# Kernel optimization log

Hardware: AMD Instinct MI355X
Metric: run time of the kernel (lower is better)

Reference implementation:

```python
import jax, jax.numpy as jnp
import numpy as np

B, L_IN, D_MODEL, CONV_D, KSIZE = 16, 512, 384, 1536, 3
MEL_MAX = 4096
LN_EPS = 1e-5


def _conv1d_same(h, w, b):
    # h: [B, C_in, L], w: [C_out, C_in, K] -> [B, C_out, L]
    y = jax.lax.conv_general_dilated(h, w, window_strides=(1,), padding='SAME',
                                     dimension_numbers=('NCH', 'OIH', 'NCH'))
    return y + b[None, :, None]


def _layernorm(x, g, b):
    m = jnp.mean(x, -1, keepdims=True)
    v = jnp.mean((x - m) ** 2, -1, keepdims=True)
    return (x - m) * jax.lax.rsqrt(v + LN_EPS) * g + b


def _ffn(x, wa, ba, wb, bb):
    # Conv1D_FFT: conv(d_model->conv_d) ReLU conv(conv_d->d_model) ReLU
    h = jnp.transpose(x, (0, 2, 1))
    h = jax.nn.relu(_conv1d_same(h, wa, ba))
    h = jax.nn.relu(_conv1d_same(h, wb, bb))
    return jnp.transpose(h, (0, 2, 1))


def _dur_pred(x, w1, b1, w2, b2, g1, be1, w3, b3, w4, b4, g2, be2, wl, bl):
    h = _ffn(x, w1, b1, w2, b2)
    h = _layernorm(h, g1, be1)  # dropout is identity at eval
    h = _ffn(h, w3, b3, w4, b4)
    h = _layernorm(h, g2, be2)
    return (h @ wl + bl)[..., 0]  # [B, L_in], squeeze(-1)


def _length_regulate(x, dur, mel_max_len):
    # Equivalent to alignment @ x where alignment[b,t,j]=1 iff cum[b,j-1] <= t < cum[b,j],
    # padded with zeros out to mel_max_len (original pads output to mel_max_len).
    cum = jnp.cumsum(dur, axis=-1)                        # [B, L_in]
    total = cum[:, -1]                                    # [B]
    t = jnp.arange(mel_max_len, dtype=cum.dtype)          # [T]
    idx = jax.vmap(lambda c: jnp.searchsorted(c, t, side='right'))(cum)  # [B, T]
    idx = jnp.minimum(idx, x.shape[1] - 1)
    out = jnp.take_along_axis(x, idx[:, :, None], axis=1)  # [B, T, D]
    mask = (t[None, :] < total[:, None])[..., None]
    return out * mask


def setup_inputs() -> dict:
    key = jax.random.key(0)
    ks = jax.random.split(key, 8)
    def nrm(k, shape):
        return jax.random.normal(k, shape, jnp.float32) * 0.02
    return {
        'x': jax.random.normal(ks[0], (B, L_IN, D_MODEL), jnp.float32),
        'target': jax.random.randint(ks[1], (B, L_IN), 0, 8, jnp.int32),
        'mel_max_len': MEL_MAX,
        'w1': nrm(ks[2], (CONV_D, D_MODEL, KSIZE)), 'b1': jnp.zeros((CONV_D,), jnp.float32),
        'w2': nrm(ks[3], (D_MODEL, CONV_D, KSIZE)), 'b2': jnp.zeros((D_MODEL,), jnp.float32),
        'g1': jnp.ones((D_MODEL,), jnp.float32), 'be1': jnp.zeros((D_MODEL,), jnp.float32),
        'w3': nrm(ks[4], (CONV_D, D_MODEL, KSIZE)), 'b3': jnp.zeros((CONV_D,), jnp.float32),
        'w4': nrm(ks[5], (D_MODEL, CONV_D, KSIZE)), 'b4': jnp.zeros((D_MODEL,), jnp.float32),
        'g2': jnp.ones((D_MODEL,), jnp.float32), 'be2': jnp.zeros((D_MODEL,), jnp.float32),
        'wl': nrm(ks[6], (D_MODEL, 1)), 'bl': jnp.zeros((1,), jnp.float32),
    }


def reference(x, target, mel_max_len, w1, b1, w2, b2, g1, be1, w3, b3, w4, b4, g2, be2, wl, bl):
    dur_preds = _dur_pred(x, w1, b1, w2, b2, g1, be1, w3, b3, w4, b4, g2, be2, wl, bl)
    output = _length_regulate(x, target, mel_max_len)
    return (output, dur_preds)
```

## Files before the change

### kernel.cpp

```cpp
#include <hip/hip_runtime.h>
#include <hip/hip_bf16.h>
#include <cstddef>
#include <cstdint>

#define NB 16
#define LIN 512
#define DM 384
#define DC 1536
#define MELMAX 4096
#define LN_EPS 1e-5f

typedef __bf16 bf16x8 __attribute__((ext_vector_type(8)));
typedef float f32x4 __attribute__((ext_vector_type(4)));

#define GL2LDS(gp, lp)                                                                \
    __builtin_amdgcn_global_load_lds((const __attribute__((address_space(1))) void*)(gp), \
                                     (__attribute__((address_space(3))) void*)(lp), 16, 0, 0)

__device__ __forceinline__ float wred(float v) {
#pragma unroll
    for (int m = 32; m >= 1; m >>= 1) v += __shfl_xor(v, m, 64);
    return v;
}

__device__ __forceinline__ unsigned short f2bf(float f) {
    __hip_bfloat16 h = __float2bfloat16(f);
    return *reinterpret_cast<unsigned short*>(&h);
}

__device__ __forceinline__ float bf2f(unsigned short u) {
    return __uint_as_float(((unsigned)u) << 16);
}


__global__ void cumsum_kernel(const int* __restrict__ tgt, int* __restrict__ cum) {
    __shared__ int s[LIN];
    const int b = blockIdx.x, tid = threadIdx.x;
    s[tid] = tgt[b * LIN + tid];
    __syncthreads();
    for (int off = 1; off < LIN; off <<= 1) {
        int v = (tid >= off) ? s[tid - off] : 0;
        __syncthreads();
        s[tid] += v;
        __syncthreads();
    }
    cum[b * LIN + tid] = s[tid];
}


__global__ __launch_bounds__(256) void gather_kernel(const float* __restrict__ x,
                                                     const int* __restrict__ cum,
                                                     float* __restrict__ out) {
    const int wid = (blockIdx.x * 256 + threadIdx.x) >> 6;
    const int lane = threadIdx.x & 63;
    const int b = wid >> 12;
    const int t = wid & (MELMAX - 1);
    const int* c = cum + b * LIN;
    const int total = c[LIN - 1];
    float4* orow = reinterpret_cast<float4*>(out + ((size_t)b * MELMAX + t) * DM);
    if (t < total) {
        int lo = 0, hi = LIN;
        while (lo < hi) { int mid = (lo + hi) >> 1; if (c[mid] > t) hi = mid; else lo = mid + 1; }
        const int idx = lo < (LIN - 1) ? lo : (LIN - 1);
        const float4* xrow = reinterpret_cast<const float4*>(x + ((size_t)b * LIN + idx) * DM);
#pragma unroll
        for (int j = 0; j < 2; ++j) {
            const int p = lane + 64 * j;
            if (p < DM / 4) orow[p] = xrow[p];
        }
    } else {
        const float4 z = make_float4(0.f, 0.f, 0.f, 0.f);
#pragma unroll
        for (int j = 0; j < 2; ++j) {
            const int p = lane + 64 * j;
            if (p < DM / 4) orow[p] = z;
        }
    }
}


__global__ void zpad_kernel(unsigned short* __restrict__ p, int rowlen) {
    const int b = blockIdx.x >> 1;
    const int row = (blockIdx.x & 1) ? (LIN + 1) : 0;
    unsigned short* base = p + ((size_t)b * (LIN + 2) + row) * rowlen;
    for (int c = threadIdx.x; c < rowlen; c += 256) base[c] = 0;
}

__global__ void cast_x_kernel(const float* __restrict__ x, unsigned short* __restrict__ xb) {
    const int idx = blockIdx.x * 256 + threadIdx.x;
    const int total = NB * LIN * DM / 4;
    if (idx >= total) return;
    const float4 v = reinterpret_cast<const float4*>(x)[idx];
    const int e = idx * 4;
    const int b = e / (LIN * DM);
    const int rem = e - b * (LIN * DM);
    const int l = rem / DM;
    const int c = rem - l * DM;
    ushort4 o;
    o.x = f2bf(v.x); o.y = f2bf(v.y); o.z = f2bf(v.z); o.w = f2bf(v.w);
    *reinterpret_cast<ushort4*>(xb + ((size_t)b * (LIN + 2) + l + 1) * DM + c) = o;
}

template <int CI, int CO>
__global__ void wcast_kernel(const float* __restrict__ w, unsigned short* __restrict__ wg) {
    const int idx = blockIdx.x * 256 + threadIdx.x;
    if (idx >= CO * CI) return;
    const int co = idx / CI;
    const int ci = idx - co * CI;
    const float* p = w + (size_t)idx * 3;
    unsigned short* o = wg + (size_t)co * (3 * CI) + ci;
    o[0 * CI] = f2bf(p[0]);
    o[1 * CI] = f2bf(p[1]);
    o[2 * CI] = f2bf(p[2]);
}


template <int CI, int CO, int BN>
__global__ __launch_bounds__(256, 2) void conv_mfma_kernel(const unsigned short* __restrict__ in,
                                                           const unsigned short* __restrict__ wg,
                                                           const float* __restrict__ bias,
                                                           unsigned short* __restrict__ out) {
    constexpr int BM = 128, BK = 32;
    constexpr int KC = CI / BK;
    constexpr int AROWS = BM + 16;
    constexpr int AGRP = AROWS / 16;
    constexpr int BGRP = 3 * BN / 16;
    constexpr int GPT = BN / 16;
    constexpr int NW_N = BN / 32;
    constexpr int NT = CO / BN;
    constexpr int MT = LIN / BM;

    __shared__ __align__(16) unsigned short As[AROWS * BK];
    __shared__ __align__(16) unsigned short Bs[3 * BN * BK];

    const int orig = blockIdx.x, nwg = gridDim.x;
    const int q = nwg >> 3, r = nwg & 7, xcd = orig & 7, o = orig >> 3;
    const int wgid = (xcd < r ? xcd * (q + 1) : r * (q + 1) + (xcd - r) * q) + o;

    const int mg = wgid / NT;
    const int nt = wgid - mg * NT;
    const int b = mg >> 2;
    const int l0 = (mg & (MT - 1)) * BM;
    const int n0 = nt * BN;

    const int tid = threadIdx.x;
    const int lane = tid & 63;
    const int wv = tid >> 6;
    const int wr = wv >> 1, wc = wv & 1;

    const unsigned short* inb = in + (size_t)b * (LIN + 2) * CI;

    f32x4 acc[4][NW_N];
#pragma unroll
    for (int m = 0; m < 4; ++m)
#pragma unroll
        for (int n = 0; n < NW_N; ++n) acc[m][n] = (f32x4){0.f, 0.f, 0.f, 0.f};

    const int lrow = lane >> 2;
    const int lch = lane & 3;

    for (int kb = 0; kb < KC; ++kb) {
        const int kin = kb * BK;
        const unsigned short* abase = inb + (size_t)l0 * CI + kin + lch * 8;
        for (int g = wv; g < AGRP; g += 4) {
            GL2LDS(abase + (size_t)(g * 16 + lrow) * CI, As + g * 512);
        }
        for (int g2 = wv; g2 < BGRP; g2 += 4) {
            const int t = g2 / GPT, gr = g2 - t * GPT;
            const unsigned short* gb =
                wg + (size_t)(n0 + gr * 16 + lrow) * (3 * CI) + (size_t)t * CI + kin + lch * 8;
            GL2LDS(gb, Bs + g2 * 512);
        }
        __syncthreads();
        {
            const int fr = lane & 15, kg = lane >> 4;
#pragma unroll
            for (int t = 0; t < 3; ++t) {
                bf16x8 aF[4], bF[NW_N];
#pragma unroll
                for (int m = 0; m < 4; ++m)
                    aF[m] = *reinterpret_cast<const bf16x8*>(
                        As + (t + wr * 64 + m * 16 + fr) * BK + kg * 8);
#pragma unroll
                for (int n = 0; n < NW_N; ++n)
                    bF[n] = *reinterpret_cast<const bf16x8*>(
                        Bs + ((size_t)t * BN + wc * (BN / 2) + n * 16 + fr) * BK + kg * 8);
#pragma unroll
                for (int m = 0; m < 4; ++m)
#pragma unroll
                    for (int n = 0; n < NW_N; ++n)
                        acc[m][n] = __builtin_amdgcn_mfma_f32_16x16x32_bf16(aF[m], bF[n], acc[m][n], 0, 0, 0);
            }
        }
        __syncthreads();
    }

    const int fr = lane & 15, fq = lane >> 4;
    float bv[NW_N];
#pragma unroll
    for (int n = 0; n < NW_N; ++n) bv[n] = bias[n0 + wc * (BN / 2) + n * 16 + fr];
    unsigned short* outb = out + (size_t)b * (LIN + 2) * CO;
#pragma unroll
    for (int m = 0; m < 4; ++m)
#pragma unroll
        for (int qy = 0; qy < 4; ++qy) {
            const int grow = l0 + wr * 64 + m * 16 + fq * 4 + qy + 1;
            unsigned short* orow = outb + (size_t)grow * CO + n0 + wc * (BN / 2) + fr;
#pragma unroll
            for (int n = 0; n < NW_N; ++n) {
                const float v = fmaxf(acc[m][n][qy] + bv[n], 0.f);
                orow[n * 16] = f2bf(v);
            }
        }
}


__global__ void ln_kernel(unsigned short* __restrict__ h, const float* __restrict__ g,
                          const float* __restrict__ be) {
    const int row = blockIdx.x, lane = threadIdx.x;
    const int b = row >> 9, l = row & (LIN - 1);
    unsigned short* hr = h + ((size_t)b * (LIN + 2) + l + 1) * DM;
    float v[6];
    float s = 0.f;
#pragma unroll
    for (int j = 0; j < 6; ++j) { v[j] = bf2f(hr[lane + 64 * j]); s += v[j]; }
    s = wred(s);
    const float mean = s * (1.f / DM);
    float vs = 0.f;
#pragma unroll
    for (int j = 0; j < 6; ++j) { const float d = v[j] - mean; vs += d * d; }
    vs = wred(vs);
    const float rstd = rsqrtf(vs * (1.f / DM) + LN_EPS);
#pragma unroll
    for (int j = 0; j < 6; ++j) {
        const int c = lane + 64 * j;
        hr[c] = f2bf((v[j] - mean) * rstd * g[c] + be[c]);
    }
}


__global__ void ln_linear_kernel(const unsigned short* __restrict__ h, const float* __restrict__ g,
                                 const float* __restrict__ be, const float* __restrict__ wl,
                                 const float* __restrict__ bl, float* __restrict__ dur) {
    const int row = blockIdx.x, lane = threadIdx.x;
    const int b = row >> 9, l = row & (LIN - 1);
    const unsigned short* hr = h + ((size_t)b * (LIN + 2) + l + 1) * DM;
    float v[6];
    float s = 0.f;
#pragma unroll
    for (int j = 0; j < 6; ++j) { v[j] = bf2f(hr[lane + 64 * j]); s += v[j]; }
    s = wred(s);
    const float mean = s * (1.f / DM);
    float vs = 0.f;
#pragma unroll
    for (int j = 0; j < 6; ++j) { const float d = v[j] - mean; vs += d * d; }
    vs = wred(vs);
    const float rstd = rsqrtf(vs * (1.f / DM) + LN_EPS);
    float dot = 0.f;
#pragma unroll
    for (int j = 0; j < 6; ++j) {
        const int c = lane + 64 * j;
        dot += ((v[j] - mean) * rstd * g[c] + be[c]) * wl[c];
    }
    dot = wred(dot);
    if (lane == 0) dur[row] = dot + bl[0];
}


extern "C" void kernel_launch(void* const* d_in, const int* in_sizes, int n_in,
                              void* d_out, int out_size, void* d_ws, size_t ws_size,
                              hipStream_t stream) {
    const float* x   = (const float*)d_in[0];
    const int*   tgt = (const int*)d_in[1];
    const float* w1  = (const float*)d_in[3];
    const float* b1  = (const float*)d_in[4];
    const float* w2  = (const float*)d_in[5];
    const float* b2  = (const float*)d_in[6];
    const float* g1  = (const float*)d_in[7];
    const float* be1 = (const float*)d_in[8];
    const float* w3  = (const float*)d_in[9];
    const float* b3  = (const float*)d_in[10];
    const float* w4  = (const float*)d_in[11];
    const float* b4  = (const float*)d_in[12];
    const float* g2  = (const float*)d_in[13];
    const float* be2 = (const float*)d_in[14];
    const float* wl  = (const float*)d_in[15];
    const float* bl  = (const float*)d_in[16];

    float* out = (float*)d_out;
    float* dur = out + (size_t)NB * MELMAX * DM;

    unsigned short* ws = (unsigned short*)d_ws;
    unsigned short* xb   = ws;
    unsigned short* hbig = xb + (size_t)NB * (LIN + 2) * DM;
    unsigned short* h2b  = hbig + (size_t)NB * (LIN + 2) * DC;
    unsigned short* wg1  = h2b + (size_t)NB * (LIN + 2) * DM;
    unsigned short* wg2  = wg1 + (size_t)DC * 3 * DM;
    unsigned short* wg3  = wg2 + (size_t)DM * 3 * DC;
    unsigned short* wg4  = wg3 + (size_t)DC * 3 * DM;
    int* cum = (int*)(wg4 + (size_t)DM * 3 * DC);

    cumsum_kernel<<<NB, LIN, 0, stream>>>(tgt, cum);
    gather_kernel<<<(NB * MELMAX) / 4, 256, 0, stream>>>(x, cum, out);

    zpad_kernel<<<NB * 2, 256, 0, stream>>>(xb, DM);
    zpad_kernel<<<NB * 2, 256, 0, stream>>>(hbig, DC);
    zpad_kernel<<<NB * 2, 256, 0, stream>>>(h2b, DM);
    cast_x_kernel<<<(NB * LIN * DM / 4 + 255) / 256, 256, 0, stream>>>(x, xb);
    wcast_kernel<DM, DC><<<(DC * DM + 255) / 256, 256, 0, stream>>>(w1, wg1);
    wcast_kernel<DC, DM><<<(DM * DC + 255) / 256, 256, 0, stream>>>(w2, wg2);
    wcast_kernel<DM, DC><<<(DC * DM + 255) / 256, 256, 0, stream>>>(w3, wg3);
    wcast_kernel<DC, DM><<<(DM * DC + 255) / 256, 256, 0, stream>>>(w4, wg4);

    conv_mfma_kernel<DM, DC, 128><<<NB * (LIN / 128) * (DC / 128), 256, 0, stream>>>(xb, wg1, b1, hbig);
    conv_mfma_kernel<DC, DM, 64><<<NB * (LIN / 128) * (DM / 64), 256, 0, stream>>>(hbig, wg2, b2, h2b);
    ln_kernel<<<NB * LIN, 64, 0, stream>>>(h2b, g1, be1);
    conv_mfma_kernel<DM, DC, 128><<<NB * (LIN / 128) * (DC / 128), 256, 0, stream>>>(h2b, wg3, b3, hbig);
    conv_mfma_kernel<DC, DM, 64><<<NB * (LIN / 128) * (DM / 64), 256, 0, stream>>>(hbig, wg4, b4, xb);
    ln_linear_kernel<<<NB * LIN, 64, 0, stream>>>(xb, g2, be2, wl, bl, dur);
}
```

Before: 242.6 us.

## Double-buffer LDS tiles in conv MFMA kernel and merge setup launches

The conv MFMA kernel now keeps two LDS buffers for the A and B tiles, so global-to-LDS loads for the next K block are issued before computing on the current one, and one of the two barriers per K step is removed. The three zero-pad launches and the four weight-cast launches are each merged into a single kernel to cut launch overhead. Double buffering doubles LDS use per block, which may lower occupancy below the two blocks per CU the launch bounds target.

```diff
diff --git a/kernel.cpp b/kernel.cpp
--- a/kernel.cpp
+++ b/kernel.cpp
@@ -79,11 +79,15 @@
 }
 
 
-__global__ void zpad_kernel(unsigned short* __restrict__ p, int rowlen) {
-    const int b = blockIdx.x >> 1;
-    const int row = (blockIdx.x & 1) ? (LIN + 1) : 0;
-    unsigned short* base = p + ((size_t)b * (LIN + 2) + row) * rowlen;
-    for (int c = threadIdx.x; c < rowlen; c += 256) base[c] = 0;
+__global__ void zpad3_kernel(unsigned short* __restrict__ xb, unsigned short* __restrict__ hb,
+                             unsigned short* __restrict__ h2) {
+    const int i = blockIdx.x;
+    const int buf = i >> 5, rem = i & 31;
+    const int b = rem >> 1, row = (rem & 1) ? (LIN + 1) : 0;
+    unsigned short* p = buf == 0 ? xb : (buf == 1 ? hb : h2);
+    const int rl = buf == 1 ? DC : DM;
+    unsigned short* base = p + ((size_t)b * (LIN + 2) + row) * rl;
+    for (int c = threadIdx.x; c < rl; c += 256) base[c] = 0;
 }
 
 __global__ void cast_x_kernel(const float* __restrict__ x, unsigned short* __restrict__ xb) {
@@ -101,14 +105,19 @@
     *reinterpret_cast<ushort4*>(xb + ((size_t)b * (LIN + 2) + l + 1) * DM + c) = o;
 }
 
-template <int CI, int CO>
-__global__ void wcast_kernel(const float* __restrict__ w, unsigned short* __restrict__ wg) {
+__global__ void wcast_all_kernel(const float* __restrict__ w1, const float* __restrict__ w2,
+                                 const float* __restrict__ w3, const float* __restrict__ w4,
+                                 unsigned short* __restrict__ o1, unsigned short* __restrict__ o2,
+                                 unsigned short* __restrict__ o3, unsigned short* __restrict__ o4) {
     const int idx = blockIdx.x * 256 + threadIdx.x;
-    if (idx >= CO * CI) return;
-    const int co = idx / CI;
-    const int ci = idx - co * CI;
+    if (idx >= DC * DM) return;
+    const int which = blockIdx.y;
+    const float* w = which == 0 ? w1 : which == 1 ? w2 : which == 2 ? w3 : w4;
+    unsigned short* gg = which == 0 ? o1 : which == 1 ? o2 : which == 2 ? o3 : o4;
+    const int CI = (which == 0 || which == 2) ? DM : DC;
+    const int co = idx / CI, ci = idx - co * CI;
     const float* p = w + (size_t)idx * 3;
-    unsigned short* o = wg + (size_t)co * (3 * CI) + ci;
+    unsigned short* o = gg + (size_t)co * (3 * CI) + ci;
     o[0 * CI] = f2bf(p[0]);
     o[1 * CI] = f2bf(p[1]);
     o[2 * CI] = f2bf(p[2]);
@@ -124,14 +133,14 @@
     constexpr int KC = CI / BK;
     constexpr int AROWS = BM + 16;
     constexpr int AGRP = AROWS / 16;
-    constexpr int BGRP = 3 * BN / 16;
     constexpr int GPT = BN / 16;
+    constexpr int BGRP = 3 * GPT;
     constexpr int NW_N = BN / 32;
     constexpr int NT = CO / BN;
     constexpr int MT = LIN / BM;
 
-    __shared__ __align__(16) unsigned short As[AROWS * BK];
-    __shared__ __align__(16) unsigned short Bs[3 * BN * BK];
+    __shared__ __align__(16) unsigned short As[2][AROWS * BK];
+    __shared__ __align__(16) unsigned short Bs[2][3 * BN * BK];
 
     const int orig = blockIdx.x, nwg = gridDim.x;
     const int q = nwg >> 3, r = nwg & 7, xcd = orig & 7, o = orig >> 3;
@@ -158,44 +167,64 @@
 
     const int lrow = lane >> 2;
     const int lch = lane & 3;
-
-    for (int kb = 0; kb < KC; ++kb) {
-        const int kin = kb * BK;
-        const unsigned short* abase = inb + (size_t)l0 * CI + kin + lch * 8;
-        for (int g = wv; g < AGRP; g += 4) {
-            GL2LDS(abase + (size_t)(g * 16 + lrow) * CI, As + g * 512);
+    const int fr = lane & 15, kg = lane >> 4;
+
+    const unsigned short* aroot = inb + (size_t)l0 * CI + lch * 8;
+    const unsigned short* broot = wg + (size_t)n0 * (3 * CI) + lch * 8;
+
+#define STAGE(c, kb)                                                                      \
+    do {                                                                                  \
+        const unsigned short* abase = aroot + (kb) * BK;                                  \
+        for (int g = wv; g < AGRP; g += 4)                                                \
+            GL2LDS(abase + (size_t)(g * 16 + lrow) * CI, &As[c][g * 512]);                \
+        const unsigned short* bbase = broot + (kb) * BK;                                  \
+        for (int g2 = wv; g2 < BGRP; g2 += 4) {                                           \
+            const int t = g2 / GPT, gr = g2 - t * GPT;                                    \
+            GL2LDS(bbase + (size_t)(gr * 16 + lrow) * (3 * CI) + (size_t)t * CI,          \
+                   &Bs[c][g2 * 512]);                                                     \
+        }                                                                                 \
+    } while (0)
+
+#define COMPUTE(c)                                                                        \
+    do {                                                                                  \
+        _Pragma("unroll")                                                                 \
+        for (int t = 0; t < 3; ++t) {                                                     \
+            bf16x8 aF[4], bF[NW_N];                                                       \
+            _Pragma("unroll")                                                             \
+            for (int m = 0; m < 4; ++m)                                                   \
+                aF[m] = *reinterpret_cast<const bf16x8*>(                                 \
+                    &As[c][(t + wr * 64 + m * 16 + fr) * BK + kg * 8]);                   \
+            _Pragma("unroll")                                                             \
+            for (int n = 0; n < NW_N; ++n)                                                \
+                bF[n] = *reinterpret_cast<const bf16x8*>(                                 \
+                    &Bs[c][(t * BN + wc * (BN / 2) + n * 16 + fr) * BK + kg * 8]);        \
+            _Pragma("unroll")                                                             \
+            for (int m = 0; m < 4; ++m)                                                   \
+                _Pragma("unroll")                                                         \
+                for (int n = 0; n < NW_N; ++n)                                            \
+                    acc[m][n] =                                                           \
+                        __builtin_amdgcn_mfma_f32_16x16x32_bf16(aF[m], bF[n], acc[m][n],  \
+                                                                0, 0, 0);                 \
+        }                                                                                 \
+    } while (0)
+
+    STAGE(0, 0);
+    __syncthreads();
+#pragma unroll 1
+    for (int kb = 0; kb < KC; kb += 2) {
+        if (kb + 1 < KC) STAGE(1, kb + 1);
+        COMPUTE(0);
+        __syncthreads();
+        if (kb + 2 < KC) STAGE(0, kb + 2);
+        if (kb + 1 < KC) {
+            COMPUTE(1);
+            __syncthreads();
         }
-        for (int g2 = wv; g2 < BGRP; g2 += 4) {
-            const int t = g2 / GPT, gr = g2 - t * GPT;
-            const unsigned short* gb =
-                wg + (size_t)(n0 + gr * 16 + lrow) * (3 * CI) + (size_t)t * CI + kin + lch * 8;
-            GL2LDS(gb, Bs + g2 * 512);
-        }
-        __syncthreads();
-        {
-            const int fr = lane & 15, kg = lane >> 4;
-#pragma unroll
-            for (int t = 0; t < 3; ++t) {
-                bf16x8 aF[4], bF[NW_N];
-#pragma unroll
-                for (int m = 0; m < 4; ++m)
-                    aF[m] = *reinterpret_cast<const bf16x8*>(
-                        As + (t + wr * 64 + m * 16 + fr) * BK + kg * 8);
-#pragma unroll
-                for (int n = 0; n < NW_N; ++n)
-                    bF[n] = *reinterpret_cast<const bf16x8*>(
-                        Bs + ((size_t)t * BN + wc * (BN / 2) + n * 16 + fr) * BK + kg * 8);
-#pragma unroll
-                for (int m = 0; m < 4; ++m)
-#pragma unroll
-                    for (int n = 0; n < NW_N; ++n)
-                        acc[m][n] = __builtin_amdgcn_mfma_f32_16x16x32_bf16(aF[m], bF[n], acc[m][n], 0, 0, 0);
-            }
-        }
-        __syncthreads();
-    }
-
-    const int fr = lane & 15, fq = lane >> 4;
+    }
+#undef STAGE
+#undef COMPUTE
+
+    const int fq = lane >> 4;
     float bv[NW_N];
 #pragma unroll
     for (int n = 0; n < NW_N; ++n) bv[n] = bias[n0 + wc * (BN / 2) + n * 16 + fr];
@@ -303,14 +332,10 @@
     cumsum_kernel<<<NB, LIN, 0, stream>>>(tgt, cum);
     gather_kernel<<<(NB * MELMAX) / 4, 256, 0, stream>>>(x, cum, out);
 
-    zpad_kernel<<<NB * 2, 256, 0, stream>>>(xb, DM);
-    zpad_kernel<<<NB * 2, 256, 0, stream>>>(hbig, DC);
-    zpad_kernel<<<NB * 2, 256, 0, stream>>>(h2b, DM);
+    zpad3_kernel<<<NB * 2 * 3, 256, 0, stream>>>(xb, hbig, h2b);
     cast_x_kernel<<<(NB * LIN * DM / 4 + 255) / 256, 256, 0, stream>>>(x, xb);
-    wcast_kernel<DM, DC><<<(DC * DM + 255) / 256, 256, 0, stream>>>(w1, wg1);
-    wcast_kernel<DC, DM><<<(DM * DC + 255) / 256, 256, 0, stream>>>(w2, wg2);
-    wcast_kernel<DM, DC><<<(DC * DM + 255) / 256, 256, 0, stream>>>(w3, wg3);
-    wcast_kernel<DC, DM><<<(DM * DC + 255) / 256, 256, 0, stream>>>(w4, wg4);
+    wcast_all_kernel<<<dim3((DC * DM + 255) / 256, 4), 256, 0, stream>>>(w1, w2, w3, w4,
+                                                                         wg1, wg2, wg3, wg4);
 
     conv_mfma_kernel<DM, DC, 128><<<NB * (LIN / 128) * (DC / 128), 256, 0, stream>>>(xb, wg1, b1, hbig);
     conv_mfma_kernel<DC, DM, 64><<<NB * (LIN / 128) * (DM / 64), 256, 0, stream>>>(hbig, wg2, b2, h2b);
```

Measured after the change: 231.9 us. -4.4%, faster.
